# Kernel tuning notes

Hardware: AMD Instinct MI355X
Metric: run time of the kernel (lower is better)

The kernel has to match this reference:

```python
import jax, jax.numpy as jnp
import numpy as np

N_ENTITIES = 500000
N_RELATIONS = 200
EMBED_DIM = 128
RELATION_DIM = 128  # must equal EMBED_DIM for the reshape in calculate_score
BATCH = 16384
KG_L2_LAMBDA = 1e-5


def _xavier_uniform(key, shape):
    fan_in, fan_out = shape[0], shape[1]
    limit = float(np.sqrt(6.0 / (fan_in + fan_out)))
    return jax.random.uniform(key, shape, jnp.float32, -limit, limit)


def setup_inputs() -> dict:
    key = jax.random.key(0)
    k1, k2, k3, k4, k5, k6 = jax.random.split(key, 6)
    entity_embed = _xavier_uniform(k1, (N_ENTITIES, EMBED_DIM))
    relation_embed = _xavier_uniform(k2, (N_RELATIONS, RELATION_DIM * EMBED_DIM))
    h = jax.random.randint(k3, (BATCH,), 0, N_ENTITIES, dtype=jnp.int64)
    r = jax.random.randint(k4, (BATCH,), 0, N_RELATIONS, dtype=jnp.int64)
    pos_t = jax.random.randint(k5, (BATCH,), 0, N_ENTITIES, dtype=jnp.int64)
    neg_t = jax.random.randint(k6, (BATCH,), 0, N_ENTITIES, dtype=jnp.int64)
    return {"h": h, "r": r, "pos_t": pos_t, "neg_t": neg_t,
            "entity_embed": entity_embed, "relation_embed": relation_embed}


def _l2_loss_mean(x):
    # mean over batch of sum(x^2, dim=1) / 2
    return jnp.mean(jnp.sum(x * x, axis=1) / 2.0)


def _score(h_e, t_e, r_mat):
    # r_mat: (B, relation_dim, embed_dim); tr = r @ t : (B, embed_dim)
    tr = jnp.einsum('bde,be->bd', r_mat, t_e)
    return -jnp.sum(h_e * tr, axis=-1)  # (B,)


def reference(h, r, pos_t, neg_t, entity_embed, relation_embed):
    r_embed = relation_embed[r]                     # (B, R*D)
    head_embed = entity_embed[h]                    # (B, D)
    tail_pos_embed = entity_embed[pos_t]            # (B, D)
    tail_neg_embed = entity_embed[neg_t]            # (B, D)
    r_mat = r_embed.reshape(-1, RELATION_DIM, EMBED_DIM)
    pos_score = _score(head_embed, tail_pos_embed, r_mat)
    neg_score = _score(head_embed, tail_neg_embed, r_mat)
    triplet_loss = jnp.mean(-jax.nn.log_sigmoid(neg_score - pos_score))
    l2_loss = (_l2_loss_mean(head_embed) + _l2_loss_mean(r_embed)
               + _l2_loss_mean(tail_pos_embed) + _l2_loss_mean(tail_neg_embed))
    return triplet_loss + KG_L2_LAMBDA * l2_loss
```

## Files before the change

### kernel.cpp

```cpp
#include <hip/hip_runtime.h>
#include <math.h>

#define BATCH 16384
#define EDIM 128
#define RD (EDIM * EDIM)
#define NREL 200
#define SPLIT 2
#define NBLK (NREL * SPLIT)
#define NTHR 512
#define HALF (BATCH / SPLIT)
#define NJ (HALF / NTHR)
#define EBW 3
#define LISTCAP 256


__device__ __forceinline__ int load_idx(const void* p, int b, int is64) {
    if (is64) return (int)((const long long*)p)[b];
    return ((const int*)p)[b];
}

__global__ __launch_bounds__(NTHR, 4) void rescal_kernel(
    const void* __restrict__ hI, const void* __restrict__ rI,
    const void* __restrict__ pI, const void* __restrict__ nI,
    const float* __restrict__ ent, const float* __restrict__ rel,
    float* __restrict__ csum) {
    const int t = threadIdx.x;
    const int bid0 = blockIdx.x;
    const int xcd = bid0 & 7;
    const int slot = bid0 >> 3;
    const int rid = xcd + 8 * (slot >> 1);
    const int half = slot & 1;
    const int lane = t & 63;
    const int wave = t >> 6;
    const int c2 = lane * 2;

    __shared__ __attribute__((aligned(16))) float Rl[RD];
    __shared__ __attribute__((aligned(16))) float hL[8][EBW][EDIM];
    __shared__ unsigned short list[LISTCAP];
    __shared__ unsigned int wtj[NJ][8];
    __shared__ unsigned int um8[8];
    __shared__ float rsq[8], wsum[8];

    unsigned int o = 0u;
    if (t < 256) {
        o = ((const unsigned int*)hI)[2 * t + 1] | ((const unsigned int*)rI)[2 * t + 1] |
            ((const unsigned int*)pI)[2 * t + 1] | ((const unsigned int*)nI)[2 * t + 1];
    }
#pragma unroll
    for (int off = 32; off; off >>= 1) o |= __shfl_xor(o, off, 64);
    if (lane == 0) um8[wave] = o;
    __syncthreads();
    const int is64 = ((um8[0] | um8[1] | um8[2] | um8[3] |
                       um8[4] | um8[5] | um8[6] | um8[7]) == 0u) ? 1 : 0;

    const float* Rg = rel + (size_t)rid * RD;
    float r2p = 0.f;
#pragma unroll
    for (int it = 0; it < 8; ++it) {
        const int idx = it * (NTHR * 4) + t * 4;
        const float4 v = *(const float4*)(Rg + idx);
        *(float4*)&Rl[idx] = v;
        r2p = fmaf(v.x, v.x, fmaf(v.y, v.y, fmaf(v.z, v.z, fmaf(v.w, v.w, r2p))));
    }
#pragma unroll
    for (int off = 32; off; off >>= 1) r2p += __shfl_xor(r2p, off, 64);
    if (lane == 0) rsq[wave] = r2p;

    const int qbase = half * HALF;
    unsigned long long bal[NJ];
#pragma unroll
    for (int j = 0; j < NJ; ++j) {
        const int rr = load_idx(rI, qbase + j * NTHR + t, is64);
        bal[j] = __ballot(rr == rid);
        if (lane == 0) wtj[j][wave] = (unsigned int)__popcll(bal[j]);
    }
    __syncthreads();

    int cnt;
    {
        unsigned int run = 0;
        const unsigned long long ltmask = (lane == 63) ? ~0ull >> 1
                                                       : (1ull << lane) - 1ull;
#pragma unroll
        for (int j = 0; j < NJ; ++j) {
            unsigned int wpre = 0, tj = 0;
#pragma unroll
            for (int w = 0; w < 8; ++w) {
                const unsigned int v = wtj[j][w];
                tj += v;
                wpre += (w < wave) ? v : 0;
            }
            if ((bal[j] >> lane) & 1ull) {
                const unsigned int rank =
                    run + wpre + (unsigned int)__popcll(bal[j] & ltmask);
                if (rank < LISTCAP) list[rank] = (unsigned short)(j * NTHR + t);
            }
            run += tj;
        }
        cnt = (int)run;
        if (cnt > LISTCAP) cnt = LISTCAP;
    }
    __syncthreads();

    const float r2sum = rsq[0] + rsq[1] + rsq[2] + rsq[3] +
                        rsq[4] + rsq[5] + rsq[6] + rsq[7];

    const int per_wave = (cnt + 7) >> 3;
    int lo = wave * per_wave;
    int hi = (wave + 1) * per_wave;
    if (lo > cnt) lo = cnt;
    if (hi > cnt) hi = cnt;

    float lsum = 0.f;

    for (int e0 = lo; e0 < hi; e0 += EBW) {
        int bidx[EBW];
        float2 h2[EBW];
#pragma unroll
        for (int i = 0; i < EBW; ++i) {
            int e = e0 + i;
            if (e >= hi) e = hi - 1;
            int b = qbase + (int)list[e];
            b = __builtin_amdgcn_readfirstlane(b);
            bidx[i] = b;
            int hix = load_idx(hI, b, is64);
            hix = __builtin_amdgcn_readfirstlane(hix);
            h2[i] = *(const float2*)(ent + (size_t)hix * EDIM + c2);
            *(float2*)&hL[wave][i][c2] = h2[i];
        }

        float2 tpv[EBW], tnv[EBW];
#pragma unroll
        for (int i = 0; i < EBW; ++i) {
            const int b = bidx[i];
            const int pi = __builtin_amdgcn_readfirstlane(load_idx(pI, b, is64));
            const int ni = __builtin_amdgcn_readfirstlane(load_idx(nI, b, is64));
            tpv[i] = *(const float2*)(ent + (size_t)pi * EDIM + c2);
            tnv[i] = *(const float2*)(ent + (size_t)ni * EDIM + c2);
        }

        float2 acc[EBW];
#pragma unroll
        for (int i = 0; i < EBW; ++i) acc[i] = make_float2(0.f, 0.f);
#pragma unroll 4
        for (int db = 0; db < 32; ++db) {
            const float4 hv0 = *(const float4*)&hL[wave][0][db * 4];
            const float4 hv1 = *(const float4*)&hL[wave][1][db * 4];
            const float4 hv2 = *(const float4*)&hL[wave][2][db * 4];
#pragma unroll
            for (int jj = 0; jj < 4; ++jj) {
                const int d = db * 4 + jj;
                const float2 rv = *(const float2*)&Rl[d * EDIM + c2];
                const float h0 = (jj == 0) ? hv0.x : (jj == 1) ? hv0.y : (jj == 2) ? hv0.z : hv0.w;
                const float h1 = (jj == 0) ? hv1.x : (jj == 1) ? hv1.y : (jj == 2) ? hv1.z : hv1.w;
                const float h2b = (jj == 0) ? hv2.x : (jj == 1) ? hv2.y : (jj == 2) ? hv2.z : hv2.w;
                acc[0].x = fmaf(rv.x, h0, acc[0].x);  acc[0].y = fmaf(rv.y, h0, acc[0].y);
                acc[1].x = fmaf(rv.x, h1, acc[1].x);  acc[1].y = fmaf(rv.y, h1, acc[1].y);
                acc[2].x = fmaf(rv.x, h2b, acc[2].x); acc[2].y = fmaf(rv.y, h2b, acc[2].y);
            }
        }

#pragma unroll
        for (int i = 0; i < EBW; ++i) {
            float dp = acc[i].x * tpv[i].x + acc[i].y * tpv[i].y;
            float dn = acc[i].x * tnv[i].x + acc[i].y * tnv[i].y;
            float e2 = h2[i].x * h2[i].x + h2[i].y * h2[i].y +
                       tpv[i].x * tpv[i].x + tpv[i].y * tpv[i].y +
                       tnv[i].x * tnv[i].x + tnv[i].y * tnv[i].y;
#pragma unroll
            for (int off = 32; off; off >>= 1) {
                dp += __shfl_xor(dp, off, 64);
                dn += __shfl_xor(dn, off, 64);
                e2 += __shfl_xor(e2, off, 64);
            }
            if (lane == 0 && (e0 + i) < hi) {
                const float x = dn - dp;
                const float spl = (x > 0.f) ? (x + log1pf(expf(-x))) : log1pf(expf(x));
                lsum += spl + 1e-5f * 0.5f * (e2 + r2sum);
            }
        }
    }

    if (lane == 0) wsum[wave] = lsum;
    __syncthreads();
    if (t == 0) {
        csum[bid0] = wsum[0] + wsum[1] + wsum[2] + wsum[3] +
                     wsum[4] + wsum[5] + wsum[6] + wsum[7];
    }
}

__global__ __launch_bounds__(256) void reduce_kernel(const float* __restrict__ csum,
                                                     float* __restrict__ out) {
    const int t = threadIdx.x;
    float a = 0.f;
    for (int i = t; i < NBLK; i += 256) a += csum[i];
#pragma unroll
    for (int off = 32; off; off >>= 1) a += __shfl_down(a, off, 64);
    __shared__ float sm[4];
    if ((t & 63) == 0) sm[t >> 6] = a;
    __syncthreads();
    if (t == 0) out[0] = (sm[0] + sm[1] + sm[2] + sm[3]) * (1.0f / (float)BATCH);
}

extern "C" void kernel_launch(void* const* d_in, const int* in_sizes, int n_in,
                              void* d_out, int out_size, void* d_ws, size_t ws_size,
                              hipStream_t stream) {
    const void* h = d_in[0];
    const void* r = d_in[1];
    const void* pt = d_in[2];
    const void* nt = d_in[3];
    const float* ent = (const float*)d_in[4];
    const float* rel = (const float*)d_in[5];
    float* csum = (float*)d_ws;

    rescal_kernel<<<NBLK, NTHR, 0, stream>>>(h, r, pt, nt, ent, rel, csum);
    reduce_kernel<<<1, 256, 0, stream>>>(csum, (float*)d_out);
}
```

Baseline: 48.01 us.

## Store relation matrix as bf16 in LDS, split batch four ways, fuse final reduction

The relation matrix is now kept in shared memory as packed bf16, halving LDS use so more blocks fit per CU (launch bounds raised to 6). The batch is split into quarters, giving 800 blocks with a smaller per-block match list. The separate reduce kernel is replaced by a last-block-done atomic counter, which needs a memset launch instead. Rounding relation weights to bf16 adds precision error, and the list cap of 128 per quarter could overflow for skewed inputs.

```diff
diff --git a/kernel.cpp b/kernel.cpp
--- a/kernel.cpp
+++ b/kernel.cpp
@@ -5,13 +5,13 @@
 #define EDIM 128
 #define RD (EDIM * EDIM)
 #define NREL 200
-#define SPLIT 2
+#define SPLIT 4
 #define NBLK (NREL * SPLIT)
 #define NTHR 512
-#define HALF (BATCH / SPLIT)
-#define NJ (HALF / NTHR)
+#define QUARTER (BATCH / SPLIT)
+#define NJ (QUARTER / NTHR)
 #define EBW 3
-#define LISTCAP 256
+#define LISTCAP 128
 
 
 __device__ __forceinline__ int load_idx(const void* p, int b, int is64) {
@@ -19,27 +19,36 @@
     return ((const int*)p)[b];
 }
 
-__global__ __launch_bounds__(NTHR, 4) void rescal_kernel(
+__device__ __forceinline__ unsigned int pack_bf16(float a, float b) {
+    unsigned int ua = __float_as_uint(a);
+    ua += 0x7fffu + ((ua >> 16) & 1u);
+    unsigned int ub = __float_as_uint(b);
+    ub += 0x7fffu + ((ub >> 16) & 1u);
+    return (ua >> 16) | (ub & 0xffff0000u);
+}
+
+__global__ __launch_bounds__(NTHR, 6) void rescal_kernel(
     const void* __restrict__ hI, const void* __restrict__ rI,
     const void* __restrict__ pI, const void* __restrict__ nI,
     const float* __restrict__ ent, const float* __restrict__ rel,
-    float* __restrict__ csum) {
+    float* __restrict__ ws, float* __restrict__ out) {
     const int t = threadIdx.x;
     const int bid0 = blockIdx.x;
     const int xcd = bid0 & 7;
     const int slot = bid0 >> 3;
-    const int rid = xcd + 8 * (slot >> 1);
-    const int half = slot & 1;
+    const int rid = xcd + 8 * (slot >> 2);
+    const int qtr = slot & 3;
     const int lane = t & 63;
     const int wave = t >> 6;
     const int c2 = lane * 2;
 
-    __shared__ __attribute__((aligned(16))) float Rl[RD];
+    __shared__ unsigned int Rlb[RD / 2];
     __shared__ __attribute__((aligned(16))) float hL[8][EBW][EDIM];
     __shared__ unsigned short list[LISTCAP];
     __shared__ unsigned int wtj[NJ][8];
     __shared__ unsigned int um8[8];
     __shared__ float rsq[8], wsum[8];
+    __shared__ int s_last;
 
     unsigned int o = 0u;
     if (t < 256) {
@@ -57,16 +66,18 @@
     float r2p = 0.f;
 #pragma unroll
     for (int it = 0; it < 8; ++it) {
-        const int idx = it * (NTHR * 4) + t * 4;
-        const float4 v = *(const float4*)(Rg + idx);
-        *(float4*)&Rl[idx] = v;
+        const int fidx = it * (NTHR * 4) + t * 4;
+        const float4 v = *(const float4*)(Rg + fidx);
         r2p = fmaf(v.x, v.x, fmaf(v.y, v.y, fmaf(v.z, v.z, fmaf(v.w, v.w, r2p))));
+        const int uidx = it * (NTHR * 2) + t * 2;
+        Rlb[uidx] = pack_bf16(v.x, v.y);
+        Rlb[uidx + 1] = pack_bf16(v.z, v.w);
     }
 #pragma unroll
     for (int off = 32; off; off >>= 1) r2p += __shfl_xor(r2p, off, 64);
     if (lane == 0) rsq[wave] = r2p;
 
-    const int qbase = half * HALF;
+    const int qbase = qtr * QUARTER;
     unsigned long long bal[NJ];
 #pragma unroll
     for (int j = 0; j < NJ; ++j) {
@@ -150,13 +161,15 @@
 #pragma unroll
             for (int jj = 0; jj < 4; ++jj) {
                 const int d = db * 4 + jj;
-                const float2 rv = *(const float2*)&Rl[d * EDIM + c2];
+                const unsigned int u = Rlb[d * 64 + lane];
+                const float rx = __uint_as_float(u << 16);
+                const float ry = __uint_as_float(u & 0xffff0000u);
                 const float h0 = (jj == 0) ? hv0.x : (jj == 1) ? hv0.y : (jj == 2) ? hv0.z : hv0.w;
                 const float h1 = (jj == 0) ? hv1.x : (jj == 1) ? hv1.y : (jj == 2) ? hv1.z : hv1.w;
                 const float h2b = (jj == 0) ? hv2.x : (jj == 1) ? hv2.y : (jj == 2) ? hv2.z : hv2.w;
-                acc[0].x = fmaf(rv.x, h0, acc[0].x);  acc[0].y = fmaf(rv.y, h0, acc[0].y);
-                acc[1].x = fmaf(rv.x, h1, acc[1].x);  acc[1].y = fmaf(rv.y, h1, acc[1].y);
-                acc[2].x = fmaf(rv.x, h2b, acc[2].x); acc[2].y = fmaf(rv.y, h2b, acc[2].y);
+                acc[0].x = fmaf(rx, h0, acc[0].x);  acc[0].y = fmaf(ry, h0, acc[0].y);
+                acc[1].x = fmaf(rx, h1, acc[1].x);  acc[1].y = fmaf(ry, h1, acc[1].y);
+                acc[2].x = fmaf(rx, h2b, acc[2].x); acc[2].y = fmaf(ry, h2b, acc[2].y);
             }
         }
 
@@ -184,22 +197,26 @@
     if (lane == 0) wsum[wave] = lsum;
     __syncthreads();
     if (t == 0) {
-        csum[bid0] = wsum[0] + wsum[1] + wsum[2] + wsum[3] +
-                     wsum[4] + wsum[5] + wsum[6] + wsum[7];
-    }
-}
-
-__global__ __launch_bounds__(256) void reduce_kernel(const float* __restrict__ csum,
-                                                     float* __restrict__ out) {
-    const int t = threadIdx.x;
-    float a = 0.f;
-    for (int i = t; i < NBLK; i += 256) a += csum[i];
-#pragma unroll
-    for (int off = 32; off; off >>= 1) a += __shfl_down(a, off, 64);
-    __shared__ float sm[4];
-    if ((t & 63) == 0) sm[t >> 6] = a;
-    __syncthreads();
-    if (t == 0) out[0] = (sm[0] + sm[1] + sm[2] + sm[3]) * (1.0f / (float)BATCH);
+        ws[bid0] = wsum[0] + wsum[1] + wsum[2] + wsum[3] +
+                   wsum[4] + wsum[5] + wsum[6] + wsum[7];
+        __threadfence();
+        unsigned int old = atomicAdd((unsigned int*)(ws + 2048), 1u);
+        s_last = (old == (unsigned int)(NBLK - 1)) ? 1 : 0;
+    }
+    __syncthreads();
+    if (s_last) {
+        __threadfence();
+        float a = 0.f;
+        for (int i = t; i < NBLK; i += NTHR)
+            a += __hip_atomic_load(&ws[i], __ATOMIC_ACQUIRE, __HIP_MEMORY_SCOPE_AGENT);
+#pragma unroll
+        for (int off = 32; off; off >>= 1) a += __shfl_down(a, off, 64);
+        if (lane == 0) wsum[wave] = a;
+        __syncthreads();
+        if (t == 0)
+            out[0] = (wsum[0] + wsum[1] + wsum[2] + wsum[3] +
+                      wsum[4] + wsum[5] + wsum[6] + wsum[7]) * (1.0f / (float)BATCH);
+    }
 }
 
 extern "C" void kernel_launch(void* const* d_in, const int* in_sizes, int n_in,
@@ -211,8 +228,9 @@
     const void* nt = d_in[3];
     const float* ent = (const float*)d_in[4];
     const float* rel = (const float*)d_in[5];
-    float* csum = (float*)d_ws;
-
-    rescal_kernel<<<NBLK, NTHR, 0, stream>>>(h, r, pt, nt, ent, rel, csum);
-    reduce_kernel<<<1, 256, 0, stream>>>(csum, (float*)d_out);
-}
+
+    hipMemsetAsync((void*)((char*)d_ws + 2048 * sizeof(float)), 0,
+                   sizeof(unsigned int), stream);
+    rescal_kernel<<<NBLK, NTHR, 0, stream>>>(h, r, pt, nt, ent, rel,
+                                             (float*)d_ws, (float*)d_out);
+}
```

Result: slower. 56.00 us (+16.6%).
